# Performance work log

Measured on AMD Instinct MI355X. Metric: run time of the kernel, lower is better.

Reference implementation:

```python
import jax, jax.numpy as jnp
import numpy as np

N_NODES = 100000
N_EDGES = 3200000
IN_DIM = 4
BIG = 32
HID = 2
BN_EPS = 1e-5


def _lin_init(key, fan_in, fan_out):
    k1, k2 = jax.random.split(key)
    bound = 1.0 / np.sqrt(fan_in)
    W = jax.random.uniform(k1, (fan_in, fan_out), minval=-bound, maxval=bound, dtype=jnp.float32)
    b = jax.random.uniform(k2, (fan_out,), minval=-bound, maxval=bound, dtype=jnp.float32)
    return W, b


def setup_inputs() -> dict:
    key = jax.random.key(0)
    ks = jax.random.split(key, 12)
    x = jax.random.normal(ks[0], (N_NODES, IN_DIM), dtype=jnp.float32)
    edge_index = jax.random.randint(ks[1], (2, N_EDGES), 0, N_NODES, dtype=jnp.int32)
    eps_noise = jax.random.normal(ks[2], (N_NODES, HID), dtype=jnp.float32)
    # batchnorm affine params
    bn_gamma = jnp.ones((IN_DIM,), jnp.float32)
    bn_beta = jnp.zeros((IN_DIM,), jnp.float32)
    # encoder EdgeConv MLP: 2*IN_DIM -> BIG -> BIG
    eW1, eb1 = _lin_init(ks[3], 2 * IN_DIM, BIG)
    eW2, eb2 = _lin_init(ks[4], BIG, BIG)
    # mu / logvar heads
    mW, mb = _lin_init(ks[5], BIG, HID)
    vW, vb = _lin_init(ks[6], BIG, HID)
    # decoder EdgeConv MLP: 2*HID -> BIG -> BIG -> IN_DIM
    dW1, db1 = _lin_init(ks[7], 2 * HID, BIG)
    dW2, db2 = _lin_init(ks[8], BIG, BIG)
    dW3, db3 = _lin_init(ks[9], BIG, IN_DIM)
    return dict(x=x, edge_index=edge_index, eps_noise=eps_noise,
                bn_gamma=bn_gamma, bn_beta=bn_beta,
                eW1=eW1, eb1=eb1, eW2=eW2, eb2=eb2,
                mW=mW, mb=mb, vW=vW, vb=vb,
                dW1=dW1, db1=db1, dW2=dW2, db2=db2, dW3=dW3, db3=db3)


def _segment_mean(msgs, tgt, n):
    s = jax.ops.segment_sum(msgs, tgt, num_segments=n)
    c = jax.ops.segment_sum(jnp.ones((msgs.shape[0],), msgs.dtype), tgt, num_segments=n)
    return s / jnp.maximum(c, 1.0)[:, None]


def _edge_conv(x, edge_index, mlp):
    # PyG EdgeConv: h_i = mean_{j->i} nn([x_i, x_j - x_i])
    src, tgt = edge_index[0], edge_index[1]
    x_i = x[tgt]                      # [E, F]
    x_j = x[src]                      # [E, F]
    feat = jnp.concatenate([x_i, x_j - x_i], axis=-1)  # [E, 2F]
    msg = mlp(feat)                   # [E, F_out]
    return _segment_mean(msg, tgt, x.shape[0])


def reference(x, edge_index, eps_noise, bn_gamma, bn_beta,
              eW1, eb1, eW2, eb2, mW, mb, vW, vb,
              dW1, db1, dW2, db2, dW3, db3):
    # BatchNorm1d (training mode: batch statistics, biased variance)
    mean = jnp.mean(x, axis=0)
    var = jnp.var(x, axis=0)
    xn = (x - mean) * jax.lax.rsqrt(var + BN_EPS) * bn_gamma + bn_beta

    enc_mlp = lambda f: jax.nn.relu(jax.nn.relu(f @ eW1 + eb1) @ eW2 + eb2)
    h = _edge_conv(xn, edge_index, enc_mlp)           # [N, BIG]

    mu = h @ mW + mb                                  # [N, HID]
    log_var = h @ vW + vb                             # [N, HID]
    z = mu + eps_noise * jnp.exp(0.5 * log_var)       # reparameterize

    dec_mlp = lambda f: jax.nn.relu(jax.nn.relu(f @ dW1 + db1) @ dW2 + db2) @ dW3 + db3
    out = _edge_conv(z, edge_index, dec_mlp)          # [N, IN_DIM]
    return out, mu, log_var
```

## Files before the change

kernel.cpp:

```cpp
#include <hip/hip_runtime.h>
#include <math.h>

#define N_NODES 100000
#define N_EDGES 3200000
#define NBLK_EDGE ((N_EDGES + 255) / 256)
#define NBLK_NODE ((N_NODES + 255) / 256)

#define NB 64
#define NBUCK ((N_NODES + NB - 1) / NB)
#define NSLICE 256
#define SLICE (N_EDGES / NSLICE)
#define P2 2048

typedef _Float16 h2f16 __attribute__((ext_vector_type(2)));
typedef __fp16 f16x8 __attribute__((ext_vector_type(8)));
typedef float f32x4 __attribute__((ext_vector_type(4)));
typedef unsigned u32x4 __attribute__((ext_vector_type(4)));

#define PK_ENC_A2 0
#define PK_DEC_A2 512
#define PK_ENC_A1 1024
#define PK_DEC_A1 1536
#define PK_ENC_HA 2048
#define PK_DEC_HA 2304
#define PK_TOTAL 2560

__device__ __forceinline__ h2f16 mkh2(float a, float b) {
  h2f16 h;
  h.x = (_Float16)a;
  h.y = (_Float16)b;
  return h;
}
__device__ __forceinline__ float fdot2(h2f16 a, h2f16 b, float c) {
  return __builtin_amdgcn_fdot2(a, b, c, false);
}
__device__ __forceinline__ h2f16 pk(float a, float b) {
  auto r = __builtin_amdgcn_cvt_pkrtz(a, b);
  return __builtin_bit_cast(h2f16, r);
}
__device__ __forceinline__ unsigned h2u(h2f16 h) {
  return __builtin_bit_cast(unsigned, h);
}
__device__ __forceinline__ f32x4 mfma16(f16x8 a, f16x8 b, f32x4 c) {
  return __builtin_amdgcn_mfma_f32_16x16x32_f16(a, b, c, 0, 0, 0);
}

__global__ __launch_bounds__(256) void pack_weights(
    const float* __restrict__ eW1, const float* __restrict__ eW2,
    const float* __restrict__ mW, const float* __restrict__ vW,
    const float* __restrict__ dW1, const float* __restrict__ dW2,
    const float* __restrict__ dW3, h2f16* __restrict__ wpk) {
  int t = threadIdx.x;
  for (int i = t; i < 512; i += 256) {
    int tl = i >> 8, rest = i & 255, lane = rest >> 2, p = rest & 3;
    int q = lane >> 4, c = lane & 15;
    int out = 16 * tl + c;
    int k0 = (p < 2) ? (4 * q + 2 * p) : (16 + 4 * q + 2 * (p - 2));
    wpk[PK_ENC_A2 + i] = mkh2(eW2[k0 * 32 + out], eW2[(k0 + 1) * 32 + out]);
    wpk[PK_DEC_A2 + i] = mkh2(dW2[k0 * 32 + out], dW2[(k0 + 1) * 32 + out]);
  }
  for (int i = t; i < 512; i += 256) {
    int tl = i >> 8, rest = i & 255, lane = rest >> 2, p = rest & 3;
    int q = lane >> 4, c = lane & 15;
    int out = 16 * tl + c;
    int k0 = 8 * q + 2 * p;
    float w0e = (k0 < 8) ? eW1[k0 * 32 + out] : 0.0f;
    float w1e = (k0 + 1 < 8) ? eW1[(k0 + 1) * 32 + out] : 0.0f;
    float w0d = (k0 < 4) ? dW1[k0 * 32 + out] : 0.0f;
    float w1d = (k0 + 1 < 4) ? dW1[(k0 + 1) * 32 + out] : 0.0f;
    wpk[PK_ENC_A1 + i] = mkh2(w0e, w1e);
    wpk[PK_DEC_A1 + i] = mkh2(w0d, w1d);
  }
  for (int i = t; i < 256; i += 256) {
    int lane = i >> 2, p = i & 3;
    int q = lane >> 4, c = lane & 15;
    int d0 = (p < 2) ? (4 * q + 2 * p) : (16 + 4 * q + 2 * (p - 2));
    int d1 = d0 + 1;
    float e0 = 0.f, e1 = 0.f, g0 = 0.f, g1 = 0.f;
    if (c < 4) {
      e0 = (c < 2) ? mW[d0 * 2 + c] : vW[d0 * 2 + (c - 2)];
      e1 = (c < 2) ? mW[d1 * 2 + c] : vW[d1 * 2 + (c - 2)];
      g0 = dW3[d0 * 4 + c];
      g1 = dW3[d1 * 4 + c];
    }
    wpk[PK_ENC_HA + i] = mkh2(e0, e1);
    wpk[PK_DEC_HA + i] = mkh2(g0, g1);
  }
}

__global__ void bn_reduce(const float4* __restrict__ x, float* __restrict__ bns) {
  float s0 = 0, s1 = 0, s2 = 0, s3 = 0, q0 = 0, q1 = 0, q2 = 0, q3 = 0;
  for (int i = blockIdx.x * blockDim.x + threadIdx.x; i < N_NODES;
       i += gridDim.x * blockDim.x) {
    float4 v = x[i];
    s0 += v.x; s1 += v.y; s2 += v.z; s3 += v.w;
    q0 += v.x * v.x; q1 += v.y * v.y; q2 += v.z * v.z; q3 += v.w * v.w;
  }
#pragma unroll
  for (int o = 32; o; o >>= 1) {
    s0 += __shfl_down(s0, o); s1 += __shfl_down(s1, o);
    s2 += __shfl_down(s2, o); s3 += __shfl_down(s3, o);
    q0 += __shfl_down(q0, o); q1 += __shfl_down(q1, o);
    q2 += __shfl_down(q2, o); q3 += __shfl_down(q3, o);
  }
  __shared__ float red[4][8];
  int w = threadIdx.x >> 6;
  if ((threadIdx.x & 63) == 0) {
    red[w][0] = s0; red[w][1] = s1; red[w][2] = s2; red[w][3] = s3;
    red[w][4] = q0; red[w][5] = q1; red[w][6] = q2; red[w][7] = q3;
  }
  __syncthreads();
  if (threadIdx.x < 8) {
    float acc = red[0][threadIdx.x] + red[1][threadIdx.x] +
                red[2][threadIdx.x] + red[3][threadIdx.x];
    atomicAdd(&bns[threadIdx.x], acc);
  }
}

__global__ void bn_final(const float* __restrict__ bns,
                         const float* __restrict__ gamma,
                         const float* __restrict__ beta,
                         float* __restrict__ ab) {
  int d = threadIdx.x;
  if (d < 4) {
    float mean = bns[d] * (1.0f / N_NODES);
    float var = bns[4 + d] * (1.0f / N_NODES) - mean * mean;
    float a = gamma[d] * rsqrtf(var + 1e-5f);
    ab[d] = a;
    ab[4 + d] = beta[d] - mean * a;
  }
}

__global__ __launch_bounds__(256) void edge_hist(const int* __restrict__ tgt,
                                                 unsigned* __restrict__ hist) {
  __shared__ unsigned h[NBUCK];
  for (int i = threadIdx.x; i < NBUCK; i += 256) h[i] = 0;
  __syncthreads();
  int e0 = blockIdx.x * SLICE;
  for (int i = threadIdx.x; i < SLICE; i += 256)
    atomicAdd(&h[((unsigned)tgt[e0 + i]) >> 6], 1u);
  __syncthreads();
  for (int i = threadIdx.x; i < NBUCK; i += 256)
    hist[(size_t)blockIdx.x * NBUCK + i] = h[i];
}

__global__ __launch_bounds__(256) void bucket_tot(const unsigned* __restrict__ hist,
                                                  unsigned* __restrict__ tot) {
  int k = blockIdx.x * 256 + threadIdx.x;
  if (k >= NBUCK) return;
  unsigned s = 0;
#pragma unroll 8
  for (int b = 0; b < NSLICE; ++b) s += hist[(size_t)b * NBUCK + k];
  tot[k] = s;
}

__global__ __launch_bounds__(1024) void bucket_start(const unsigned* __restrict__ tot,
                                                     unsigned* __restrict__ start) {
  __shared__ unsigned sa[P2], sb[P2];
  for (int k = threadIdx.x; k < P2; k += 1024)
    sa[k] = (k < NBUCK) ? tot[k] : 0u;
  __syncthreads();
  unsigned *srcp = sa, *dstp = sb;
  for (int off = 1; off < P2; off <<= 1) {
    for (int k = threadIdx.x; k < P2; k += 1024)
      dstp[k] = srcp[k] + (k >= off ? srcp[k - off] : 0u);
    __syncthreads();
    unsigned* t = srcp; srcp = dstp; dstp = t;
  }
  for (int k = threadIdx.x; k <= NBUCK; k += 1024)
    start[k] = (k == 0) ? 0u : srcp[k - 1];
}

__global__ __launch_bounds__(256) void bucket_bases(unsigned* __restrict__ hist,
                                                    const unsigned* __restrict__ start) {
  int wv = threadIdx.x >> 6, lane = threadIdx.x & 63;
  int k = blockIdx.x * 4 + wv;
  if (k >= NBUCK) return;
  unsigned v0 = hist[(size_t)(4 * lane + 0) * NBUCK + k];
  unsigned v1 = hist[(size_t)(4 * lane + 1) * NBUCK + k];
  unsigned v2 = hist[(size_t)(4 * lane + 2) * NBUCK + k];
  unsigned v3 = hist[(size_t)(4 * lane + 3) * NBUCK + k];
  unsigned p1 = v0, p2 = v0 + v1, p3 = v0 + v1 + v2;
  unsigned s = p3 + v3;
  unsigned incl = s;
#pragma unroll
  for (int off = 1; off < 64; off <<= 1) {
    unsigned t = __shfl_up(incl, off);
    incl += (lane >= off) ? t : 0u;
  }
  unsigned base = start[k] + (incl - s);
  hist[(size_t)(4 * lane + 0) * NBUCK + k] = base;
  hist[(size_t)(4 * lane + 1) * NBUCK + k] = base + p1;
  hist[(size_t)(4 * lane + 2) * NBUCK + k] = base + p2;
  hist[(size_t)(4 * lane + 3) * NBUCK + k] = base + p3;
}

__global__ __launch_bounds__(256) void edge_place(
    const int* __restrict__ src, const int* __restrict__ tgt,
    const unsigned* __restrict__ hist, const unsigned* __restrict__ start,
    unsigned* __restrict__ payload) {
  __shared__ unsigned stage[SLICE];
  __shared__ unsigned offA[NBUCK];
  __shared__ unsigned A2[NBUCK];
  int s = blockIdx.x, tid = threadIdx.x;
  for (int k = tid; k < NBUCK; k += 256) {
    unsigned gb = hist[(size_t)s * NBUCK + k];
    unsigned nb = (s == NSLICE - 1) ? start[k + 1]
                                    : hist[(size_t)(s + 1) * NBUCK + k];
    offA[k] = gb;
    A2[k] = nb - gb;
  }
  __syncthreads();
  for (int d = 1; d < NBUCK; d <<= 1) {
    unsigned tmp[7];
    int m = 0;
    for (int k = tid; k < NBUCK; k += 256, ++m)
      tmp[m] = (k >= d) ? A2[k - d] : 0u;
    __syncthreads();
    m = 0;
    for (int k = tid; k < NBUCK; k += 256, ++m) A2[k] += tmp[m];
    __syncthreads();
  }
  {
    unsigned tmp[7];
    int m = 0;
    for (int k = tid; k < NBUCK; k += 256, ++m)
      tmp[m] = (k == 0) ? 0u : A2[k - 1];
    __syncthreads();
    m = 0;
    for (int k = tid; k < NBUCK; k += 256, ++m) {
      offA[k] -= tmp[m];
      A2[k] = tmp[m];
    }
    __syncthreads();
  }
  int e0 = s * SLICE;
  for (int i = tid; i < SLICE; i += 256) {
    unsigned t = (unsigned)tgt[e0 + i];
    unsigned sr = (unsigned)src[e0 + i];
    unsigned b = t >> 6;
    unsigned lp = atomicAdd(&A2[b], 1u);
    stage[lp] = sr | ((t & 63u) << 17);
  }
  __syncthreads();
  for (int b = tid; b < NBUCK; b += 256) {
    unsigned beg = (b == 0) ? 0u : A2[b - 1];
    unsigned end = A2[b];
    unsigned go = offA[b];
    for (unsigned i = beg; i < end; ++i) payload[go + i] = stage[i];
  }
}

__global__ __launch_bounds__(256, 4) void enc_bucket(
    const float4* __restrict__ x, const unsigned* __restrict__ payload,
    const unsigned* __restrict__ start, const float* __restrict__ ab,
    const float* __restrict__ eb1, const float* __restrict__ eb2,
    const h2f16* __restrict__ wpk, float2* __restrict__ mpart,
    float2* __restrict__ vpart, float* __restrict__ cpart) {
  __shared__ float aM0[NB], aM1[NB], aV0[NB], aV1[NB], aC[NB];
  __shared__ float4 xt[NB];
  int k = blockIdx.x, node0 = k * NB, h = blockIdx.y;
  int tid = threadIdx.x, w = tid >> 6, lane = tid & 63;
  int q = lane >> 4, c = lane & 15;
  if (tid < NB) {
    int n = node0 + tid;
    aM0[tid] = 0; aM1[tid] = 0; aV0[tid] = 0; aV1[tid] = 0; aC[tid] = 0;
    xt[tid] = x[n < N_NODES ? n : 0];
  }
  __syncthreads();
  float a0 = ab[0], a1 = ab[1], a2 = ab[2], a3 = ab[3];
  float b0 = ab[4], b1 = ab[5], b2 = ab[6], b3 = ab[7];
  const u32x4* a2t = (const u32x4*)(wpk + PK_ENC_A2);
  const u32x4* a1t = (const u32x4*)(wpk + PK_ENC_A1);
  const u32x4* hat = (const u32x4*)(wpk + PK_ENC_HA);
  f16x8 A20 = __builtin_bit_cast(f16x8, a2t[lane]);
  f16x8 A21 = __builtin_bit_cast(f16x8, a2t[64 + lane]);
  f16x8 A10 = __builtin_bit_cast(f16x8, a1t[lane]);
  f16x8 A11 = __builtin_bit_cast(f16x8, a1t[64 + lane]);
  f16x8 HA = __builtin_bit_cast(f16x8, hat[lane]);
  float e1a[4], e1b[4], e2a[4], e2b[4];
#pragma unroll
  for (int r = 0; r < 4; ++r) {
    e1a[r] = eb1[4 * q + r];
    e1b[r] = eb1[16 + 4 * q + r];
    e2a[r] = eb2[4 * q + r];
    e2b[r] = eb2[16 + 4 * q + r];
  }
  unsigned s0v = start[k], s1v = start[k + 1];
  unsigned len = s1v - s0v, halfv = (len + 1) >> 1;
  unsigned lo = s0v + (h ? halfv : 0u);
  unsigned hi = h ? s1v : (s0v + halfv);
  unsigned base = lo + (unsigned)w * 32u;
  if (base < hi) {
    unsigned eA = base + (unsigned)c;
    eA = eA < hi ? eA : hi - 1u;
    unsigned eB = base + 16u + (unsigned)c;
    eB = eB < hi ? eB : hi - 1u;
    unsigned pA = payload[eA], pB = payload[eB];
    float4 xjA = x[(int)(pA & 0x1FFFFu)];
    float4 xjB = x[(int)(pB & 0x1FFFFu)];
    f32x4 zf = {0.f, 0.f, 0.f, 0.f};
    for (; base < hi; base += 128u) {
      unsigned nb = base + 128u;
      unsigned eAn = nb + (unsigned)c;
      eAn = eAn < hi ? eAn : hi - 1u;
      unsigned eBn = nb + 16u + (unsigned)c;
      eBn = eBn < hi ? eBn : hi - 1u;
      unsigned pAn = payload[eAn];
      unsigned pBn = payload[eBn];
      int ltiA = (int)(pA >> 17), ltiB = (int)(pB >> 17);
      float4 xiA = xt[ltiA], xiB = xt[ltiB];
      bool vA = (base + (unsigned)c) < hi;
      bool vB = (base + 16u + (unsigned)c) < hi;
      u32x4 fuA, fuB;
      fuA[0] = h2u(pk(fmaf(a0, xiA.x, b0), fmaf(a1, xiA.y, b1)));
      fuA[1] = h2u(pk(fmaf(a2, xiA.z, b2), fmaf(a3, xiA.w, b3)));
      fuA[2] = h2u(pk(a0 * (xjA.x - xiA.x), a1 * (xjA.y - xiA.y)));
      fuA[3] = h2u(pk(a2 * (xjA.z - xiA.z), a3 * (xjA.w - xiA.w)));
      fuB[0] = h2u(pk(fmaf(a0, xiB.x, b0), fmaf(a1, xiB.y, b1)));
      fuB[1] = h2u(pk(fmaf(a2, xiB.z, b2), fmaf(a3, xiB.w, b3)));
      fuB[2] = h2u(pk(a0 * (xjB.x - xiB.x), a1 * (xjB.y - xiB.y)));
      fuB[3] = h2u(pk(a2 * (xjB.z - xiB.z), a3 * (xjB.w - xiB.w)));
      float4 xjAn = x[(int)(pAn & 0x1FFFFu)];
      float4 xjBn = x[(int)(pBn & 0x1FFFFu)];
      f16x8 FA = __builtin_bit_cast(f16x8, fuA);
      f16x8 FB = __builtin_bit_cast(f16x8, fuB);
      f32x4 D10A = mfma16(A10, FA, zf), D11A = mfma16(A11, FA, zf);
      f32x4 D10B = mfma16(A10, FB, zf), D11B = mfma16(A11, FB, zf);
      u32x4 h1A, h1B;
      h1A[0] = h2u(pk(fmaxf(D10A[0] + e1a[0], 0.f), fmaxf(D10A[1] + e1a[1], 0.f)));
      h1A[1] = h2u(pk(fmaxf(D10A[2] + e1a[2], 0.f), fmaxf(D10A[3] + e1a[3], 0.f)));
      h1A[2] = h2u(pk(fmaxf(D11A[0] + e1b[0], 0.f), fmaxf(D11A[1] + e1b[1], 0.f)));
      h1A[3] = h2u(pk(fmaxf(D11A[2] + e1b[2], 0.f), fmaxf(D11A[3] + e1b[3], 0.f)));
      h1B[0] = h2u(pk(fmaxf(D10B[0] + e1a[0], 0.f), fmaxf(D10B[1] + e1a[1], 0.f)));
      h1B[1] = h2u(pk(fmaxf(D10B[2] + e1a[2], 0.f), fmaxf(D10B[3] + e1a[3], 0.f)));
      h1B[2] = h2u(pk(fmaxf(D11B[0] + e1b[0], 0.f), fmaxf(D11B[1] + e1b[1], 0.f)));
      h1B[3] = h2u(pk(fmaxf(D11B[2] + e1b[2], 0.f), fmaxf(D11B[3] + e1b[3], 0.f)));
      f16x8 B2A = __builtin_bit_cast(f16x8, h1A);
      f16x8 B2B = __builtin_bit_cast(f16x8, h1B);
      f32x4 C0A = mfma16(A20, B2A, zf), C1A = mfma16(A21, B2A, zf);
      f32x4 C0B = mfma16(A20, B2B, zf), C1B = mfma16(A21, B2B, zf);
      u32x4 g2A, g2B;
      g2A[0] = h2u(pk(fmaxf(C0A[0] + e2a[0], 0.f), fmaxf(C0A[1] + e2a[1], 0.f)));
      g2A[1] = h2u(pk(fmaxf(C0A[2] + e2a[2], 0.f), fmaxf(C0A[3] + e2a[3], 0.f)));
      g2A[2] = h2u(pk(fmaxf(C1A[0] + e2b[0], 0.f), fmaxf(C1A[1] + e2b[1], 0.f)));
      g2A[3] = h2u(pk(fmaxf(C1A[2] + e2b[2], 0.f), fmaxf(C1A[3] + e2b[3], 0.f)));
      g2B[0] = h2u(pk(fmaxf(C0B[0] + e2a[0], 0.f), fmaxf(C0B[1] + e2a[1], 0.f)));
      g2B[1] = h2u(pk(fmaxf(C0B[2] + e2a[2], 0.f), fmaxf(C0B[3] + e2a[3], 0.f)));
      g2B[2] = h2u(pk(fmaxf(C1B[0] + e2b[0], 0.f), fmaxf(C1B[1] + e2b[1], 0.f)));
      g2B[3] = h2u(pk(fmaxf(C1B[2] + e2b[2], 0.f), fmaxf(C1B[3] + e2b[3], 0.f)));
      f32x4 D2A = mfma16(HA, __builtin_bit_cast(f16x8, g2A), zf);
      f32x4 D2B = mfma16(HA, __builtin_bit_cast(f16x8, g2B), zf);
      if (lane < 16) {
        if (vA) {
          atomicAdd(&aM0[ltiA], D2A[0]);
          atomicAdd(&aM1[ltiA], D2A[1]);
          atomicAdd(&aV0[ltiA], D2A[2]);
          atomicAdd(&aV1[ltiA], D2A[3]);
          atomicAdd(&aC[ltiA], 1.0f);
        }
        if (vB) {
          atomicAdd(&aM0[ltiB], D2B[0]);
          atomicAdd(&aM1[ltiB], D2B[1]);
          atomicAdd(&aV0[ltiB], D2B[2]);
          atomicAdd(&aV1[ltiB], D2B[3]);
          atomicAdd(&aC[ltiB], 1.0f);
        }
      }
      pA = pAn; pB = pBn; xjA = xjAn; xjB = xjBn;
    }
  }
  __syncthreads();
  if (tid < NB) {
    int n = node0 + tid;
    if (n < N_NODES) {
      mpart[(size_t)h * N_NODES + n] = make_float2(aM0[tid], aM1[tid]);
      vpart[(size_t)h * N_NODES + n] = make_float2(aV0[tid], aV1[tid]);
      cpart[(size_t)h * N_NODES + n] = aC[tid];
    }
  }
}

__global__ __launch_bounds__(256) void node_mid(
    const float2* __restrict__ mpart, const float2* __restrict__ vpart,
    const float* __restrict__ cpart, const float* __restrict__ eps2,
    const float* __restrict__ mbias, const float* __restrict__ vbias,
    float* __restrict__ z, float* __restrict__ cntC,
    float2* __restrict__ muOut, float2* __restrict__ lvOut) {
  int n = blockIdx.x * 256 + threadIdx.x;
  if (n >= N_NODES) return;
  float2 ma = mpart[n], mb2 = mpart[N_NODES + n];
  float2 va = vpart[n], vb2 = vpart[N_NODES + n];
  float cc = cpart[n] + cpart[N_NODES + n];
  float inv = 1.0f / fmaxf(cc, 1.0f);
  float mu0 = fmaf(ma.x + mb2.x, inv, mbias[0]);
  float mu1 = fmaf(ma.y + mb2.y, inv, mbias[1]);
  float lv0 = fmaf(va.x + vb2.x, inv, vbias[0]);
  float lv1 = fmaf(va.y + vb2.y, inv, vbias[1]);
  cntC[n] = cc;
  muOut[n] = make_float2(mu0, mu1);
  lvOut[n] = make_float2(lv0, lv1);
  z[2 * n + 0] = fmaf(eps2[2 * n + 0], expf(0.5f * lv0), mu0);
  z[2 * n + 1] = fmaf(eps2[2 * n + 1], expf(0.5f * lv1), mu1);
}

__global__ __launch_bounds__(256, 4) void dec_bucket(
    const float2* __restrict__ z, const unsigned* __restrict__ payload,
    const unsigned* __restrict__ start, const float* __restrict__ db1,
    const float* __restrict__ db2, const float* __restrict__ db3,
    const h2f16* __restrict__ wpk, float4* __restrict__ opart) {
  __shared__ float aO0[NB], aO1[NB], aO2[NB], aO3[NB];
  __shared__ float2 zt[NB];
  int k = blockIdx.x, node0 = k * NB, h = blockIdx.y;
  int tid = threadIdx.x, w = tid >> 6, lane = tid & 63;
  int q = lane >> 4, c = lane & 15;
  if (tid < NB) {
    int n = node0 + tid;
    aO0[tid] = 0; aO1[tid] = 0; aO2[tid] = 0; aO3[tid] = 0;
    zt[tid] = z[n < N_NODES ? n : 0];
  }
  __syncthreads();
  const u32x4* a2t = (const u32x4*)(wpk + PK_DEC_A2);
  const u32x4* a1t = (const u32x4*)(wpk + PK_DEC_A1);
  const u32x4* hat = (const u32x4*)(wpk + PK_DEC_HA);
  f16x8 A20 = __builtin_bit_cast(f16x8, a2t[lane]);
  f16x8 A21 = __builtin_bit_cast(f16x8, a2t[64 + lane]);
  f16x8 A10 = __builtin_bit_cast(f16x8, a1t[lane]);
  f16x8 A11 = __builtin_bit_cast(f16x8, a1t[64 + lane]);
  f16x8 HA = __builtin_bit_cast(f16x8, hat[lane]);
  float e1a[4], e1b[4], e2a[4], e2b[4];
#pragma unroll
  for (int r = 0; r < 4; ++r) {
    e1a[r] = db1[4 * q + r];
    e1b[r] = db1[16 + 4 * q + r];
    e2a[r] = db2[4 * q + r];
    e2b[r] = db2[16 + 4 * q + r];
  }
  float b3_0 = db3[0], b3_1 = db3[1], b3_2 = db3[2], b3_3 = db3[3];
  unsigned s0v = start[k], s1v = start[k + 1];
  unsigned len = s1v - s0v, halfv = (len + 1) >> 1;
  unsigned lo = s0v + (h ? halfv : 0u);
  unsigned hi = h ? s1v : (s0v + halfv);
  unsigned base = lo + (unsigned)w * 32u;
  if (base < hi) {
    unsigned eA = base + (unsigned)c;
    eA = eA < hi ? eA : hi - 1u;
    unsigned eB = base + 16u + (unsigned)c;
    eB = eB < hi ? eB : hi - 1u;
    unsigned pA = payload[eA], pB = payload[eB];
    float2 zjA = z[(int)(pA & 0x1FFFFu)];
    float2 zjB = z[(int)(pB & 0x1FFFFu)];
    f32x4 zf = {0.f, 0.f, 0.f, 0.f};
    for (; base < hi; base += 128u) {
      unsigned nb = base + 128u;
      unsigned eAn = nb + (unsigned)c;
      eAn = eAn < hi ? eAn : hi - 1u;
      unsigned eBn = nb + 16u + (unsigned)c;
      eBn = eBn < hi ? eBn : hi - 1u;
      unsigned pAn = payload[eAn];
      unsigned pBn = payload[eBn];
      int ltiA = (int)(pA >> 17), ltiB = (int)(pB >> 17);
      float2 ziA = zt[ltiA], ziB = zt[ltiB];
      bool vA = (base + (unsigned)c) < hi;
      bool vB = (base + 16u + (unsigned)c) < hi;
      u32x4 fuA, fuB;
      fuA[0] = h2u(pk(ziA.x, ziA.y));
      fuA[1] = h2u(pk(zjA.x - ziA.x, zjA.y - ziA.y));
      fuA[2] = fuA[0];
      fuA[3] = fuA[1];
      fuB[0] = h2u(pk(ziB.x, ziB.y));
      fuB[1] = h2u(pk(zjB.x - ziB.x, zjB.y - ziB.y));
      fuB[2] = fuB[0];
      fuB[3] = fuB[1];
      float2 zjAn = z[(int)(pAn & 0x1FFFFu)];
      float2 zjBn = z[(int)(pBn & 0x1FFFFu)];
      f16x8 FA = __builtin_bit_cast(f16x8, fuA);
      f16x8 FB = __builtin_bit_cast(f16x8, fuB);
      f32x4 D10A = mfma16(A10, FA, zf), D11A = mfma16(A11, FA, zf);
      f32x4 D10B = mfma16(A10, FB, zf), D11B = mfma16(A11, FB, zf);
      u32x4 h1A, h1B;
      h1A[0] = h2u(pk(fmaxf(D10A[0] + e1a[0], 0.f), fmaxf(D10A[1] + e1a[1], 0.f)));
      h1A[1] = h2u(pk(fmaxf(D10A[2] + e1a[2], 0.f), fmaxf(D10A[3] + e1a[3], 0.f)));
      h1A[2] = h2u(pk(fmaxf(D11A[0] + e1b[0], 0.f), fmaxf(D11A[1] + e1b[1], 0.f)));
      h1A[3] = h2u(pk(fmaxf(D11A[2] + e1b[2], 0.f), fmaxf(D11A[3] + e1b[3], 0.f)));
      h1B[0] = h2u(pk(fmaxf(D10B[0] + e1a[0], 0.f), fmaxf(D10B[1] + e1a[1], 0.f)));
      h1B[1] = h2u(pk(fmaxf(D10B[2] + e1a[2], 0.f), fmaxf(D10B[3] + e1a[3], 0.f)));
      h1B[2] = h2u(pk(fmaxf(D11B[0] + e1b[0], 0.f), fmaxf(D11B[1] + e1b[1], 0.f)));
      h1B[3] = h2u(pk(fmaxf(D11B[2] + e1b[2], 0.f), fmaxf(D11B[3] + e1b[3], 0.f)));
      f16x8 B2A = __builtin_bit_cast(f16x8, h1A);
      f16x8 B2B = __builtin_bit_cast(f16x8, h1B);
      f32x4 C0A = mfma16(A20, B2A, zf), C1A = mfma16(A21, B2A, zf);
      f32x4 C0B = mfma16(A20, B2B, zf), C1B = mfma16(A21, B2B, zf);
      u32x4 g2A, g2B;
      g2A[0] = h2u(pk(fmaxf(C0A[0] + e2a[0], 0.f), fmaxf(C0A[1] + e2a[1], 0.f)));
      g2A[1] = h2u(pk(fmaxf(C0A[2] + e2a[2], 0.f), fmaxf(C0A[3] + e2a[3], 0.f)));
      g2A[2] = h2u(pk(fmaxf(C1A[0] + e2b[0], 0.f), fmaxf(C1A[1] + e2b[1], 0.f)));
      g2A[3] = h2u(pk(fmaxf(C1A[2] + e2b[2], 0.f), fmaxf(C1A[3] + e2b[3], 0.f)));
      g2B[0] = h2u(pk(fmaxf(C0B[0] + e2a[0], 0.f), fmaxf(C0B[1] + e2a[1], 0.f)));
      g2B[1] = h2u(pk(fmaxf(C0B[2] + e2a[2], 0.f), fmaxf(C0B[3] + e2a[3], 0.f)));
      g2B[2] = h2u(pk(fmaxf(C1B[0] + e2b[0], 0.f), fmaxf(C1B[1] + e2b[1], 0.f)));
      g2B[3] = h2u(pk(fmaxf(C1B[2] + e2b[2], 0.f), fmaxf(C1B[3] + e2b[3], 0.f)));
      f32x4 D2A = mfma16(HA, __builtin_bit_cast(f16x8, g2A), zf);
      f32x4 D2B = mfma16(HA, __builtin_bit_cast(f16x8, g2B), zf);
      if (lane < 16) {
        if (vA) {
          atomicAdd(&aO0[ltiA], D2A[0] + b3_0);
          atomicAdd(&aO1[ltiA], D2A[1] + b3_1);
          atomicAdd(&aO2[ltiA], D2A[2] + b3_2);
          atomicAdd(&aO3[ltiA], D2A[3] + b3_3);
        }
        if (vB) {
          atomicAdd(&aO0[ltiB], D2B[0] + b3_0);
          atomicAdd(&aO1[ltiB], D2B[1] + b3_1);
          atomicAdd(&aO2[ltiB], D2B[2] + b3_2);
          atomicAdd(&aO3[ltiB], D2B[3] + b3_3);
        }
      }
      pA = pAn; pB = pBn; zjA = zjAn; zjB = zjBn;
    }
  }
  __syncthreads();
  if (tid < NB) {
    int n = node0 + tid;
    if (n < N_NODES)
      opart[(size_t)h * N_NODES + n] =
          make_float4(aO0[tid], aO1[tid], aO2[tid], aO3[tid]);
  }
}

__global__ __launch_bounds__(256) void node_final(
    const float4* __restrict__ opart, const float* __restrict__ cntC,
    float4* __restrict__ outp) {
  int n = blockIdx.x * 256 + threadIdx.x;
  if (n >= N_NODES) return;
  float4 a = opart[n], b = opart[N_NODES + n];
  float inv = 1.0f / fmaxf(cntC[n], 1.0f);
  outp[n] = make_float4((a.x + b.x) * inv, (a.y + b.y) * inv,
                        (a.z + b.z) * inv, (a.w + b.w) * inv);
}

__device__ __forceinline__ void atomAddF(float* p, float v) {
  unsafeAtomicAdd(p, v);
}

__global__ __launch_bounds__(256) void enc_edge_fb(
    const float4* __restrict__ x, const int* __restrict__ esrc,
    const int* __restrict__ etgt, const float* __restrict__ ab,
    const float* __restrict__ eW1, const float* __restrict__ eb1,
    const float* __restrict__ eW2, const float* __restrict__ eb2,
    const float* __restrict__ mW, const float* __restrict__ vW,
    float* __restrict__ msum, float* __restrict__ vsum,
    float* __restrict__ cnt) {
  int e = blockIdx.x * 256 + threadIdx.x;
  if (e >= N_EDGES) return;
  int si = esrc[e], ti = etgt[e];
  float4 xi = x[ti];
  float4 xj = x[si];
  float a0 = ab[0], a1 = ab[1], a2 = ab[2], a3 = ab[3];
  float b0 = ab[4], b1 = ab[5], b2 = ab[6], b3 = ab[7];
  float feat[8];
  feat[0] = fmaf(a0, xi.x, b0);
  feat[1] = fmaf(a1, xi.y, b1);
  feat[2] = fmaf(a2, xi.z, b2);
  feat[3] = fmaf(a3, xi.w, b3);
  feat[4] = a0 * (xj.x - xi.x);
  feat[5] = a1 * (xj.y - xi.y);
  feat[6] = a2 * (xj.z - xi.z);
  feat[7] = a3 * (xj.w - xi.w);
  float h1[32];
#pragma unroll 8
  for (int j = 0; j < 32; ++j) {
    float acc = eb1[j];
#pragma unroll
    for (int kk = 0; kk < 8; ++kk) acc = fmaf(feat[kk], eW1[kk * 32 + j], acc);
    h1[j] = fmaxf(acc, 0.0f);
  }
  float m0 = 0, m1 = 0, v0 = 0, v1 = 0;
#pragma unroll 4
  for (int j = 0; j < 32; ++j) {
    float acc = eb2[j];
#pragma unroll
    for (int kk = 0; kk < 32; ++kk) acc = fmaf(h1[kk], eW2[kk * 32 + j], acc);
    float h2 = fmaxf(acc, 0.0f);
    m0 = fmaf(h2, mW[j * 2 + 0], m0);
    m1 = fmaf(h2, mW[j * 2 + 1], m1);
    v0 = fmaf(h2, vW[j * 2 + 0], v0);
    v1 = fmaf(h2, vW[j * 2 + 1], v1);
  }
  atomAddF(&msum[ti * 2 + 0], m0);
  atomAddF(&msum[ti * 2 + 1], m1);
  atomAddF(&vsum[ti * 2 + 0], v0);
  atomAddF(&vsum[ti * 2 + 1], v1);
  atomAddF(&cnt[ti], 1.0f);
}

__global__ __launch_bounds__(256) void dec_edge_fb(
    const float2* __restrict__ z, const int* __restrict__ esrc,
    const int* __restrict__ etgt, const float* __restrict__ dW1,
    const float* __restrict__ db1, const float* __restrict__ dW2,
    const float* __restrict__ db2, const float* __restrict__ dW3,
    const float* __restrict__ db3, float* __restrict__ osum) {
  int e = blockIdx.x * 256 + threadIdx.x;
  if (e >= N_EDGES) return;
  int si = esrc[e], ti = etgt[e];
  float2 zi = z[ti], zj = z[si];
  float f0 = zi.x, f1 = zi.y, f2 = zj.x - zi.x, f3 = zj.y - zi.y;
  float h1[32];
#pragma unroll 8
  for (int j = 0; j < 32; ++j) {
    float acc = db1[j];
    acc = fmaf(f0, dW1[0 * 32 + j], acc);
    acc = fmaf(f1, dW1[1 * 32 + j], acc);
    acc = fmaf(f2, dW1[2 * 32 + j], acc);
    acc = fmaf(f3, dW1[3 * 32 + j], acc);
    h1[j] = fmaxf(acc, 0.0f);
  }
  float o0 = db3[0], o1 = db3[1], o2 = db3[2], o3 = db3[3];
#pragma unroll 4
  for (int j = 0; j < 32; ++j) {
    float acc = db2[j];
#pragma unroll
    for (int kk = 0; kk < 32; ++kk) acc = fmaf(h1[kk], dW2[kk * 32 + j], acc);
    float h2 = fmaxf(acc, 0.0f);
    o0 = fmaf(h2, dW3[j * 4 + 0], o0);
    o1 = fmaf(h2, dW3[j * 4 + 1], o1);
    o2 = fmaf(h2, dW3[j * 4 + 2], o2);
    o3 = fmaf(h2, dW3[j * 4 + 3], o3);
  }
  atomAddF(&osum[4 * ti + 0], o0);
  atomAddF(&osum[4 * ti + 1], o1);
  atomAddF(&osum[4 * ti + 2], o2);
  atomAddF(&osum[4 * ti + 3], o3);
}

__global__ __launch_bounds__(256) void node_mid_fb(
    float* __restrict__ msum, float* __restrict__ vsum,
    const float* __restrict__ cnt, const float* __restrict__ eps2,
    const float* __restrict__ mb, const float* __restrict__ vb,
    float* __restrict__ z) {
  int n = blockIdx.x * 256 + threadIdx.x;
  if (n >= N_NODES) return;
  float inv = 1.0f / fmaxf(cnt[n], 1.0f);
  float mu0 = fmaf(msum[2 * n + 0], inv, mb[0]);
  float mu1 = fmaf(msum[2 * n + 1], inv, mb[1]);
  float lv0 = fmaf(vsum[2 * n + 0], inv, vb[0]);
  float lv1 = fmaf(vsum[2 * n + 1], inv, vb[1]);
  msum[2 * n + 0] = mu0;
  msum[2 * n + 1] = mu1;
  vsum[2 * n + 0] = lv0;
  vsum[2 * n + 1] = lv1;
  z[2 * n + 0] = fmaf(eps2[2 * n + 0], expf(0.5f * lv0), mu0);
  z[2 * n + 1] = fmaf(eps2[2 * n + 1], expf(0.5f * lv1), mu1);
}

__global__ __launch_bounds__(256) void node_final_fb(
    float* __restrict__ osum, const float* __restrict__ cnt) {
  int n = blockIdx.x * 256 + threadIdx.x;
  if (n >= N_NODES) return;
  float inv = 1.0f / fmaxf(cnt[n], 1.0f);
  float4* o4 = (float4*)osum;
  float4 v = o4[n];
  v.x *= inv; v.y *= inv; v.z *= inv; v.w *= inv;
  o4[n] = v;
}

extern "C" void kernel_launch(void* const* d_in, const int* in_sizes, int n_in,
                              void* d_out, int out_size, void* d_ws,
                              size_t ws_size, hipStream_t stream) {
  const float* x = (const float*)d_in[0];
  const int* ei = (const int*)d_in[1];
  const float* eps = (const float*)d_in[2];
  const float* bng = (const float*)d_in[3];
  const float* bnb = (const float*)d_in[4];
  const float* eW1 = (const float*)d_in[5];
  const float* eb1 = (const float*)d_in[6];
  const float* eW2 = (const float*)d_in[7];
  const float* eb2 = (const float*)d_in[8];
  const float* mW = (const float*)d_in[9];
  const float* mb = (const float*)d_in[10];
  const float* vW = (const float*)d_in[11];
  const float* vb = (const float*)d_in[12];
  const float* dW1 = (const float*)d_in[13];
  const float* db1 = (const float*)d_in[14];
  const float* dW2 = (const float*)d_in[15];
  const float* db2 = (const float*)d_in[16];
  const float* dW3 = (const float*)d_in[17];
  const float* db3 = (const float*)d_in[18];

  float* out = (float*)d_out;
  const size_t N = N_NODES;

  float* wsf = (float*)d_ws;
  float* bns = wsf;
  float* ab = wsf + 8;
  float* z = wsf + 16;
  float* cntC = z + 2 * N;
  float* cpart = cntC + N;
  float2* mpart = (float2*)(cpart + 2 * N);
  float2* vpart = mpart + 2 * N;
  float4* opart = (float4*)((float*)vpart + 4 * N);
  unsigned* start = (unsigned*)((float*)opart + 8 * N);
  unsigned* hist = start + (NBUCK + 1);
  unsigned* payload = hist + (size_t)NSLICE * NBUCK;
  h2f16* wpk = (h2f16*)(payload + N_EDGES);
  const size_t REQ = (16 + 21 * N) * sizeof(float) +
                     ((size_t)(NBUCK + 1) + (size_t)NSLICE * NBUCK + N_EDGES +
                      PK_TOTAL) *
                         sizeof(unsigned);

  if (ws_size >= REQ) {
    (void)hipMemsetAsync(bns, 0, 8 * sizeof(float), stream);
    pack_weights<<<1, 256, 0, stream>>>(eW1, eW2, mW, vW, dW1, dW2, dW3, wpk);
    bn_reduce<<<256, 256, 0, stream>>>((const float4*)x, bns);
    bn_final<<<1, 64, 0, stream>>>(bns, bng, bnb, ab);
    edge_hist<<<NSLICE, 256, 0, stream>>>(ei + N_EDGES, hist);
    bucket_tot<<<(NBUCK + 255) / 256, 256, 0, stream>>>(hist, payload);
    bucket_start<<<1, 1024, 0, stream>>>(payload, start);
    bucket_bases<<<(NBUCK + 3) / 4, 256, 0, stream>>>(hist, start);
    edge_place<<<NSLICE, 256, 0, stream>>>(ei, ei + N_EDGES, hist, start,
                                           payload);
    dim3 gE(NBUCK, 2);
    enc_bucket<<<gE, 256, 0, stream>>>((const float4*)x, payload, start, ab,
                                       eb1, eb2, wpk, mpart, vpart, cpart);
    node_mid<<<NBLK_NODE, 256, 0, stream>>>(mpart, vpart, cpart, eps, mb, vb,
                                            z, cntC, (float2*)(out + 4 * N),
                                            (float2*)(out + 6 * N));
    dec_bucket<<<gE, 256, 0, stream>>>((const float2*)z, payload, start, db1,
                                       db2, db3, wpk, opart);
    node_final<<<NBLK_NODE, 256, 0, stream>>>(opart, cntC, (float4*)out);
  } else {
    float* cntf = wsf + 16;
    float* zf = wsf + 16 + N;
    float* msum = out + 4 * N;
    float* vsum = out + 6 * N;
    (void)hipMemsetAsync(d_out, 0, 8 * N * sizeof(float), stream);
    (void)hipMemsetAsync(d_ws, 0, (16 + N) * sizeof(float), stream);
    bn_reduce<<<256, 256, 0, stream>>>((const float4*)x, bns);
    bn_final<<<1, 64, 0, stream>>>(bns, bng, bnb, ab);
    enc_edge_fb<<<NBLK_EDGE, 256, 0, stream>>>((const float4*)x, ei,
                                               ei + N_EDGES, ab, eW1, eb1, eW2,
                                               eb2, mW, vW, msum, vsum, cntf);
    node_mid_fb<<<NBLK_NODE, 256, 0, stream>>>(msum, vsum, cntf, eps, mb, vb,
                                               zf);
    dec_edge_fb<<<NBLK_EDGE, 256, 0, stream>>>((const float2*)zf, ei,
                                               ei + N_EDGES, dW1, db1, dW2, db2,
                                               dW3, db3, out);
    node_final_fb<<<NBLK_NODE, 256, 0, stream>>>(out, cntf);
  }
}
```

Before: 368.9 us.

## Split bucket edge ranges four ways with global atomic accumulation

Encoder and decoder bucket kernels now split each bucket's edge range into four parts instead of two. Partial sums are merged with float atomics into zeroed global buffers instead of per-split partial arrays, which shrinks the workspace and the node_mid and node_final reads. The decoder bias is moved out of the per-edge LDS atomics into node_final, and the launch bounds ask for 8 blocks per CU. This adds more blocks and parallelism at the cost of a memset, global atomic traffic and possible register pressure from the higher occupancy target.

```diff
diff --git a/kernel.cpp b/kernel.cpp
--- a/kernel.cpp
+++ b/kernel.cpp
@@ -11,6 +11,7 @@
 #define NSLICE 256
 #define SLICE (N_EDGES / NSLICE)
 #define P2 2048
+#define NSPLIT 4
 
 typedef _Float16 h2f16 __attribute__((ext_vector_type(2)));
 typedef __fp16 f16x8 __attribute__((ext_vector_type(8)));
@@ -43,6 +44,9 @@
 }
 __device__ __forceinline__ f32x4 mfma16(f16x8 a, f16x8 b, f32x4 c) {
   return __builtin_amdgcn_mfma_f32_16x16x32_f16(a, b, c, 0, 0, 0);
+}
+__device__ __forceinline__ void atomAddF(float* p, float v) {
+  unsafeAtomicAdd(p, v);
 }
 
 __global__ __launch_bounds__(256) void pack_weights(
@@ -251,15 +255,21 @@
   }
 }
 
-__global__ __launch_bounds__(256, 4) void enc_bucket(
+__global__ __launch_bounds__(256, 8) void enc_bucket(
     const float4* __restrict__ x, const unsigned* __restrict__ payload,
     const unsigned* __restrict__ start, const float* __restrict__ ab,
     const float* __restrict__ eb1, const float* __restrict__ eb2,
-    const h2f16* __restrict__ wpk, float2* __restrict__ mpart,
-    float2* __restrict__ vpart, float* __restrict__ cpart) {
+    const h2f16* __restrict__ wpk, float* __restrict__ mpart,
+    float* __restrict__ vpart, float* __restrict__ cpart) {
+  int k = blockIdx.x, node0 = k * NB, h = blockIdx.y;
+  unsigned s0v = start[k], s1v = start[k + 1];
+  unsigned len = s1v - s0v, qlen = (len + NSPLIT - 1) / NSPLIT;
+  unsigned lo = s0v + (unsigned)h * qlen;
+  unsigned hi = lo + qlen;
+  if (hi > s1v) hi = s1v;
+  if (lo >= s1v || lo >= hi) return;
   __shared__ float aM0[NB], aM1[NB], aV0[NB], aV1[NB], aC[NB];
   __shared__ float4 xt[NB];
-  int k = blockIdx.x, node0 = k * NB, h = blockIdx.y;
   int tid = threadIdx.x, w = tid >> 6, lane = tid & 63;
   int q = lane >> 4, c = lane & 15;
   if (tid < NB) {
@@ -286,10 +296,6 @@
     e2a[r] = eb2[4 * q + r];
     e2b[r] = eb2[16 + 4 * q + r];
   }
-  unsigned s0v = start[k], s1v = start[k + 1];
-  unsigned len = s1v - s0v, halfv = (len + 1) >> 1;
-  unsigned lo = s0v + (h ? halfv : 0u);
-  unsigned hi = h ? s1v : (s0v + halfv);
   unsigned base = lo + (unsigned)w * 32u;
   if (base < hi) {
     unsigned eA = base + (unsigned)c;
@@ -374,29 +380,31 @@
   if (tid < NB) {
     int n = node0 + tid;
     if (n < N_NODES) {
-      mpart[(size_t)h * N_NODES + n] = make_float2(aM0[tid], aM1[tid]);
-      vpart[(size_t)h * N_NODES + n] = make_float2(aV0[tid], aV1[tid]);
-      cpart[(size_t)h * N_NODES + n] = aC[tid];
+      atomAddF(&mpart[2 * n + 0], aM0[tid]);
+      atomAddF(&mpart[2 * n + 1], aM1[tid]);
+      atomAddF(&vpart[2 * n + 0], aV0[tid]);
+      atomAddF(&vpart[2 * n + 1], aV1[tid]);
+      atomAddF(&cpart[n], aC[tid]);
     }
   }
 }
 
 __global__ __launch_bounds__(256) void node_mid(
-    const float2* __restrict__ mpart, const float2* __restrict__ vpart,
+    const float* __restrict__ mpart, const float* __restrict__ vpart,
     const float* __restrict__ cpart, const float* __restrict__ eps2,
     const float* __restrict__ mbias, const float* __restrict__ vbias,
     float* __restrict__ z, float* __restrict__ cntC,
     float2* __restrict__ muOut, float2* __restrict__ lvOut) {
   int n = blockIdx.x * 256 + threadIdx.x;
   if (n >= N_NODES) return;
-  float2 ma = mpart[n], mb2 = mpart[N_NODES + n];
-  float2 va = vpart[n], vb2 = vpart[N_NODES + n];
-  float cc = cpart[n] + cpart[N_NODES + n];
+  float2 ma = ((const float2*)mpart)[n];
+  float2 va = ((const float2*)vpart)[n];
+  float cc = cpart[n];
   float inv = 1.0f / fmaxf(cc, 1.0f);
-  float mu0 = fmaf(ma.x + mb2.x, inv, mbias[0]);
-  float mu1 = fmaf(ma.y + mb2.y, inv, mbias[1]);
-  float lv0 = fmaf(va.x + vb2.x, inv, vbias[0]);
-  float lv1 = fmaf(va.y + vb2.y, inv, vbias[1]);
+  float mu0 = fmaf(ma.x, inv, mbias[0]);
+  float mu1 = fmaf(ma.y, inv, mbias[1]);
+  float lv0 = fmaf(va.x, inv, vbias[0]);
+  float lv1 = fmaf(va.y, inv, vbias[1]);
   cntC[n] = cc;
   muOut[n] = make_float2(mu0, mu1);
   lvOut[n] = make_float2(lv0, lv1);
@@ -404,14 +412,20 @@
   z[2 * n + 1] = fmaf(eps2[2 * n + 1], expf(0.5f * lv1), mu1);
 }
 
-__global__ __launch_bounds__(256, 4) void dec_bucket(
+__global__ __launch_bounds__(256, 8) void dec_bucket(
     const float2* __restrict__ z, const unsigned* __restrict__ payload,
     const unsigned* __restrict__ start, const float* __restrict__ db1,
-    const float* __restrict__ db2, const float* __restrict__ db3,
-    const h2f16* __restrict__ wpk, float4* __restrict__ opart) {
+    const float* __restrict__ db2, const h2f16* __restrict__ wpk,
+    float* __restrict__ opart) {
+  int k = blockIdx.x, node0 = k * NB, h = blockIdx.y;
+  unsigned s0v = start[k], s1v = start[k + 1];
+  unsigned len = s1v - s0v, qlen = (len + NSPLIT - 1) / NSPLIT;
+  unsigned lo = s0v + (unsigned)h * qlen;
+  unsigned hi = lo + qlen;
+  if (hi > s1v) hi = s1v;
+  if (lo >= s1v || lo >= hi) return;
   __shared__ float aO0[NB], aO1[NB], aO2[NB], aO3[NB];
   __shared__ float2 zt[NB];
-  int k = blockIdx.x, node0 = k * NB, h = blockIdx.y;
   int tid = threadIdx.x, w = tid >> 6, lane = tid & 63;
   int q = lane >> 4, c = lane & 15;
   if (tid < NB) {
@@ -436,11 +450,6 @@
     e2a[r] = db2[4 * q + r];
     e2b[r] = db2[16 + 4 * q + r];
   }
-  float b3_0 = db3[0], b3_1 = db3[1], b3_2 = db3[2], b3_3 = db3[3];
-  unsigned s0v = start[k], s1v = start[k + 1];
-  unsigned len = s1v - s0v, halfv = (len + 1) >> 1;
-  unsigned lo = s0v + (h ? halfv : 0u);
-  unsigned hi = h ? s1v : (s0v + halfv);
   unsigned base = lo + (unsigned)w * 32u;
   if (base < hi) {
     unsigned eA = base + (unsigned)c;
@@ -504,16 +513,16 @@
       f32x4 D2B = mfma16(HA, __builtin_bit_cast(f16x8, g2B), zf);
       if (lane < 16) {
         if (vA) {
-          atomicAdd(&aO0[ltiA], D2A[0] + b3_0);
-          atomicAdd(&aO1[ltiA], D2A[1] + b3_1);
-          atomicAdd(&aO2[ltiA], D2A[2] + b3_2);
-          atomicAdd(&aO3[ltiA], D2A[3] + b3_3);
+          atomicAdd(&aO0[ltiA], D2A[0]);
+          atomicAdd(&aO1[ltiA], D2A[1]);
+          atomicAdd(&aO2[ltiA], D2A[2]);
+          atomicAdd(&aO3[ltiA], D2A[3]);
         }
         if (vB) {
-          atomicAdd(&aO0[ltiB], D2B[0] + b3_0);
-          atomicAdd(&aO1[ltiB], D2B[1] + b3_1);
-          atomicAdd(&aO2[ltiB], D2B[2] + b3_2);
-          atomicAdd(&aO3[ltiB], D2B[3] + b3_3);
+          atomicAdd(&aO0[ltiB], D2B[0]);
+          atomicAdd(&aO1[ltiB], D2B[1]);
+          atomicAdd(&aO2[ltiB], D2B[2]);
+          atomicAdd(&aO3[ltiB], D2B[3]);
         }
       }
       pA = pAn; pB = pBn; zjA = zjAn; zjB = zjBn;
@@ -522,25 +531,29 @@
   __syncthreads();
   if (tid < NB) {
     int n = node0 + tid;
-    if (n < N_NODES)
-      opart[(size_t)h * N_NODES + n] =
-          make_float4(aO0[tid], aO1[tid], aO2[tid], aO3[tid]);
+    if (n < N_NODES) {
+      atomAddF(&opart[4 * n + 0], aO0[tid]);
+      atomAddF(&opart[4 * n + 1], aO1[tid]);
+      atomAddF(&opart[4 * n + 2], aO2[tid]);
+      atomAddF(&opart[4 * n + 3], aO3[tid]);
+    }
   }
 }
 
 __global__ __launch_bounds__(256) void node_final(
     const float4* __restrict__ opart, const float* __restrict__ cntC,
-    float4* __restrict__ outp) {
+    const float* __restrict__ db3, float4* __restrict__ outp) {
   int n = blockIdx.x * 256 + threadIdx.x;
   if (n >= N_NODES) return;
-  float4 a = opart[n], b = opart[N_NODES + n];
-  float inv = 1.0f / fmaxf(cntC[n], 1.0f);
-  outp[n] = make_float4((a.x + b.x) * inv, (a.y + b.y) * inv,
-                        (a.z + b.z) * inv, (a.w + b.w) * inv);
-}
-
-__device__ __forceinline__ void atomAddF(float* p, float v) {
-  unsafeAtomicAdd(p, v);
+  float cc = cntC[n];
+  float4 a = opart[n];
+  if (cc > 0.0f) {
+    float inv = 1.0f / cc;
+    outp[n] = make_float4(fmaf(a.x, inv, db3[0]), fmaf(a.y, inv, db3[1]),
+                          fmaf(a.z, inv, db3[2]), fmaf(a.w, inv, db3[3]));
+  } else {
+    outp[n] = make_float4(0.f, 0.f, 0.f, 0.f);
+  }
 }
 
 __global__ __launch_bounds__(256) void enc_edge_fb(
@@ -696,20 +709,21 @@
   float* z = wsf + 16;
   float* cntC = z + 2 * N;
   float* cpart = cntC + N;
-  float2* mpart = (float2*)(cpart + 2 * N);
-  float2* vpart = mpart + 2 * N;
-  float4* opart = (float4*)((float*)vpart + 4 * N);
-  unsigned* start = (unsigned*)((float*)opart + 8 * N);
+  float* mpart = cpart + N;
+  float* vpart = mpart + 2 * N;
+  float* opart = vpart + 2 * N;
+  unsigned* start = (unsigned*)(opart + 4 * N);
   unsigned* hist = start + (NBUCK + 1);
   unsigned* payload = hist + (size_t)NSLICE * NBUCK;
   h2f16* wpk = (h2f16*)(payload + N_EDGES);
-  const size_t REQ = (16 + 21 * N) * sizeof(float) +
+  const size_t REQ = (16 + 12 * N) * sizeof(float) +
                      ((size_t)(NBUCK + 1) + (size_t)NSLICE * NBUCK + N_EDGES +
                       PK_TOTAL) *
                          sizeof(unsigned);
 
   if (ws_size >= REQ) {
     (void)hipMemsetAsync(bns, 0, 8 * sizeof(float), stream);
+    (void)hipMemsetAsync(cpart, 0, 9 * N * sizeof(float), stream);
     pack_weights<<<1, 256, 0, stream>>>(eW1, eW2, mW, vW, dW1, dW2, dW3, wpk);
     bn_reduce<<<256, 256, 0, stream>>>((const float4*)x, bns);
     bn_final<<<1, 64, 0, stream>>>(bns, bng, bnb, ab);
@@ -719,15 +733,16 @@
     bucket_bases<<<(NBUCK + 3) / 4, 256, 0, stream>>>(hist, start);
     edge_place<<<NSLICE, 256, 0, stream>>>(ei, ei + N_EDGES, hist, start,
                                            payload);
-    dim3 gE(NBUCK, 2);
+    dim3 gE(NBUCK, NSPLIT);
     enc_bucket<<<gE, 256, 0, stream>>>((const float4*)x, payload, start, ab,
                                        eb1, eb2, wpk, mpart, vpart, cpart);
     node_mid<<<NBLK_NODE, 256, 0, stream>>>(mpart, vpart, cpart, eps, mb, vb,
                                             z, cntC, (float2*)(out + 4 * N),
                                             (float2*)(out + 6 * N));
     dec_bucket<<<gE, 256, 0, stream>>>((const float2*)z, payload, start, db1,
-                                       db2, db3, wpk, opart);
-    node_final<<<NBLK_NODE, 256, 0, stream>>>(opart, cntC, (float4*)out);
+                                       db2, wpk, opart);
+    node_final<<<NBLK_NODE, 256, 0, stream>>>((const float4*)opart, cntC, db3,
+                                              (float4*)out);
   } else {
     float* cntf = wsf + 16;
     float* zf = wsf + 16 + N;
```

Result: slower. 380.4 us (+3.1%).
